# Performance work log

Hardware: AMD Instinct MI355X
Metric: run time of the kernel (lower is better)

## Reference

```python
import jax, jax.numpy as jnp
import numpy as np
from jax import lax

RATE = 2
KSIZE = 3
STRIDE = 1
FUSE_K = 3
SCALE = 10.0
DN = ('NCHW', 'OIHW', 'NCHW')


def extract_patches(x, k, s):
    # x: [B,C,H,W] -> [B,nH,nW,C,k,k]  (ZeroPad2d(1) when k != 1, as in torch code)
    B, C, H, W = x.shape
    p = 0 if k == 1 else 1
    xp = jnp.pad(x, ((0, 0), (0, 0), (p, p), (p, p)))
    nH = (H + 2 * p - k) // s + 1
    nW = (W + 2 * p - k) // s + 1
    cols = [xp[:, :, di:di + s * nH:s, dj:dj + s * nW:s]
            for di in range(k) for dj in range(k)]
    pat = jnp.stack(cols, 0).reshape(k, k, B, C, nH, nW)
    return pat.transpose(2, 4, 5, 3, 0, 1)


def _fuse(y):
    # conv of the [L,L] score image with eye(FUSE_K) kernel, same padding
    # == sum of diagonal shifts of the zero-padded image
    L = y.shape[0]
    p = (FUSE_K - 1) // 2
    A = jnp.pad(y, ((p, p), (p, p)))
    out = A[0:L, 0:L]
    for d in range(1, FUSE_K):
        out = out + A[d:d + L, d:d + L]
    return out


def _per_sample(xi, wi, raw_wi, mmi, h, w):
    # xi: [C,h,w]  wi: [L,C,3,3]  raw_wi: [L,C,4,4]  mmi: [L,1,1]
    L = h * w
    norm = jnp.sqrt(jnp.sum(wi * wi, axis=(1, 2, 3), keepdims=True))
    wi_n = wi / jnp.maximum(norm, 1e-4)
    # cosine-similarity conv: [L,h,w]
    yi = lax.conv_general_dilated(xi[None], wi_n, (1, 1), ((1, 1), (1, 1)),
                                  dimension_numbers=DN)[0]
    # fuse pass 1 on [L(patch), L(spatial)]
    y = _fuse(yi.reshape(L, L))
    # transpose (h_p,w_p,h',w') -> (w_p,h_p,w',h'), fuse pass 2, transpose back
    y = y.reshape(h, w, h, w).transpose(1, 0, 3, 2).reshape(L, L)
    y = _fuse(y)
    y = y.reshape(w, h, w, h).transpose(1, 0, 3, 2).reshape(L, h, w)
    y = y * mmi
    y = jax.nn.softmax(y * SCALE, axis=0)
    y = jnp.maximum(y * mmi, 1e-8)
    # conv_transpose2d(y, raw_wi, stride=2, padding=1) as lhs-dilated conv
    Wf = raw_wi[:, :, ::-1, ::-1].transpose(1, 0, 2, 3)  # [C,L,4,4]
    out = lax.conv_general_dilated(y[None], Wf, (1, 1), ((2, 2), (2, 2)),
                                   lhs_dilation=(2, 2),
                                   dimension_numbers=DN)[0]
    return out / 4.0


def reference(x1, x2, mask):
    B, C, H, W = x1.shape
    kernel = 2 * RATE
    raw_w = extract_patches(x1, kernel, RATE * STRIDE)
    x2s = x2[:, :, ::2, ::2]          # F.interpolate scale=0.5, nearest
    h, w = x2s.shape[2], x2s.shape[3]
    L = h * w
    raw_w = raw_w.reshape(B, L, C, kernel, kernel)
    wpat = extract_patches(x2s, KSIZE, STRIDE).reshape(B, L, C, KSIZE, KSIZE)
    # mask is already [B,1,h,w]: bilinear align_corners resize to (h,w) is identity
    m = extract_patches(mask, KSIZE, STRIDE).reshape(B, L, -1).mean(axis=2)
    mm = (m == 0.0).astype(x1.dtype)[:, :, None, None]  # [B,L,1,1]
    f = lambda xi, wi, rwi, mmi: _per_sample(xi, wi, rwi, mmi, h, w)
    return jax.vmap(f)(x2s, wpat, raw_w, mm)  # [B,C,H,W]


def setup_inputs() -> dict:
    key = jax.random.key(0)
    k1, k2 = jax.random.split(key)
    x1 = jax.random.normal(k1, (2, 128, 96, 96), dtype=jnp.float32)
    x2 = jax.random.normal(k2, (2, 128, 96, 96), dtype=jnp.float32)
    mask = jnp.zeros((2, 1, 48, 48), dtype=jnp.float32)
    return {"x1": x1, "x2": x2, "mask": mask}
```

## Files before the change

### kernel.cpp

```cpp
#include <hip/hip_runtime.h>
#include <hip/hip_bf16.h>

#define Cc   128
#define Hh   96
#define hs   48
#define Ls   2304
#define CK   2048
#define KG   384

typedef __attribute__((ext_vector_type(8))) short short8;
typedef __attribute__((ext_vector_type(4))) float f32x4;

__device__ __forceinline__ unsigned short f2bf(float x) {
    unsigned int u = __float_as_uint(x);
    unsigned int r = (u + 0x7fff + ((u >> 16) & 1)) >> 16;
    return (unsigned short)r;
}

__device__ __forceinline__ f32x4 ld4u(const float* p) {
    f32x4 v; __builtin_memcpy(&v, p, 16); return v;
}

#define GLOAD_LDS16(g, l) \
    __builtin_amdgcn_global_load_lds((__attribute__((address_space(1))) const void*)(g), \
                                     (__attribute__((address_space(3))) void*)(l), 16, 0, 0)


__global__ __launch_bounds__(256) void transposePQ_k(const float* __restrict__ x2,
                                                     unsigned short* __restrict__ P,
                                                     unsigned short* __restrict__ Q,
                                                     long long sPQ, int z0) {
    const int z = z0 + blockIdx.z;
    const float* x2b = x2 + (size_t)z * Cc * Hh * Hh;
    unsigned short* Pb = P + (size_t)blockIdx.z * sPQ;
    unsigned short* Qb = Q + (size_t)blockIdx.z * sPQ;
    __shared__ float tile[64][65];
    const int c0 = blockIdx.x * 64;
    const int l0 = blockIdx.y * 64;
    const int t = threadIdx.x;
    const int lt = t & 63, cg = t >> 6;
    const int l = l0 + lt;
    const int iy = l / hs, jx = l % hs;
    const int srcoff = iy * (2 * Hh) + 2 * jx;
#pragma unroll
    for (int cc = 0; cc < 16; ++cc) {
        int c = cg * 16 + cc;
        tile[lt][c] = x2b[(size_t)(c0 + c) * (Hh * Hh) + srcoff];
    }
    __syncthreads();
    const int lr = t >> 2, seg = t & 3;
    const int lw = l0 + lr;
    short8 hv0, hv1, lv0, lv1;
#pragma unroll
    for (int k = 0; k < 8; ++k) {
        float x = tile[lr][seg * 16 + k];
        unsigned short h = f2bf(x);
        float hf = __uint_as_float((unsigned)h << 16);
        unsigned short lo = f2bf(x - hf);
        hv0[k] = (short)h; lv0[k] = (short)lo;
    }
#pragma unroll
    for (int k = 0; k < 8; ++k) {
        float x = tile[lr][seg * 16 + 8 + k];
        unsigned short h = f2bf(x);
        float hf = __uint_as_float((unsigned)h << 16);
        unsigned short lo = f2bf(x - hf);
        hv1[k] = (short)h; lv1[k] = (short)lo;
    }
    size_t rowp = (size_t)lw * KG;
    int coff = c0 + seg * 16;
    *(short8*)&Pb[rowp + coff] = hv0;        *(short8*)&Pb[rowp + coff + 8] = hv1;
    *(short8*)&Pb[rowp + 128 + coff] = lv0;  *(short8*)&Pb[rowp + 128 + coff + 8] = lv1;
    *(short8*)&Pb[rowp + 256 + coff] = hv0;  *(short8*)&Pb[rowp + 256 + coff + 8] = hv1;
    *(short8*)&Qb[rowp + coff] = hv0;        *(short8*)&Qb[rowp + coff + 8] = hv1;
    *(short8*)&Qb[rowp + 128 + coff] = hv0;  *(short8*)&Qb[rowp + 128 + coff + 8] = hv1;
    *(short8*)&Qb[rowp + 256 + coff] = lv0;  *(short8*)&Qb[rowp + 256 + coff + 8] = lv1;
}

__global__ __launch_bounds__(256) void mm_k(const float* __restrict__ mask, float* __restrict__ MM) {
    int z = blockIdx.y;
    const float* mb = mask + (size_t)z * hs * hs;
    float* MMb = MM + (size_t)z * Ls;
    int l = blockIdx.x * 256 + threadIdx.x;
    if (l >= Ls) return;
    int ly = l / hs, lx = l % hs;
    float s = 0.f;
    for (int dy = -1; dy <= 1; ++dy)
        for (int dx = -1; dx <= 1; ++dx) {
            int yy = ly + dy, xx = lx + dx;
            if ((unsigned)yy < (unsigned)hs && (unsigned)xx < (unsigned)hs) s += mb[yy * hs + xx];
        }
    float m = s * (1.0f / 9.0f);
    MMb[l] = (m == 0.0f) ? 1.0f : 0.0f;
}

__global__ __launch_bounds__(256) void taps9rn_k(const float* __restrict__ G, float* __restrict__ S,
                                                 float* __restrict__ RN, long long zsG, long long zsS, int z0) {
    const float* Gb = G + (size_t)blockIdx.z * zsG;
    float* Sb = S + (size_t)blockIdx.z * zsS;
    float* RNb = RN + (size_t)(z0 + blockIdx.z) * Ls;
    int g = blockIdx.x * 256 + threadIdx.x;
    int i = g / 576;
    int jb = (g - i * 576) * 4;
    int iy = i / hs, ix = i % hs;
    int jy = jb / hs, jx0 = jb % hs;
    f32x4 acc = {};
#pragma unroll
    for (int dy = -1; dy <= 1; ++dy) {
        int vy = ((unsigned)(iy + dy) < (unsigned)hs) && ((unsigned)(jy + dy) < (unsigned)hs);
#pragma unroll
        for (int dx = -1; dx <= 1; ++dx) {
            int vi = vy && ((unsigned)(ix + dx) < (unsigned)hs);
            int o = hs * dy + dx;
            int row = vi ? (i + o) : i;
            f32x4 v = ld4u(&Gb[(size_t)row * Ls + jb + o]);
            f32x4 m;
#pragma unroll
            for (int ln = 0; ln < 4; ++ln)
                m[ln] = (vi && ((unsigned)(jx0 + ln + dx) < (unsigned)hs)) ? 1.f : 0.f;
            acc += v * m;
        }
    }
    __builtin_memcpy(&Sb[(size_t)i * Ls + jb], &acc, 16);
    int dd = i - jb;
    if ((unsigned)dd < 4u) RNb[i] = 1.0f / fmaxf(sqrtf(acc[dd]), 1e-4f);
}

__global__ __launch_bounds__(256) void fuse12T_k(const float* __restrict__ S, const float* __restrict__ RN,
                                                 float* __restrict__ ZT, long long zsS, long long zsZT, int z0) {
    const float* Sb = S + (size_t)blockIdx.z * zsS;
    float* ZTb = ZT + (size_t)blockIdx.z * zsZT;
    const float* RNb = RN + (size_t)(z0 + blockIdx.z) * Ls;
    __shared__ float tile[64][65];
    const int i0 = blockIdx.y * 64, j0 = blockIdx.x * 64;
    const int t = threadIdx.x;
    const int jg = t & 15, tit = t >> 4;
    const int jb = j0 + jg * 4;
    const int jy0 = jb / hs, jx0 = jb % hs;

    int ccb[9]; f32x4 m4[9];
#pragma unroll
    for (int d2 = -1; d2 <= 1; ++d2) {
        int cl[4], vb[4];
#pragma unroll
        for (int ln = 0; ln < 4; ++ln) {
            int j2 = (jx0 + ln) * hs + jy0 + d2;
            int vv = ((unsigned)j2 < (unsigned)Ls) ? 1 : 0;
            int c = vv ? ((j2 % hs) * hs + j2 / hs) : 0;
            cl[ln] = c; vb[ln] = vv;
        }
        int base = 0;
#pragma unroll
        for (int ln = 0; ln < 4; ++ln) if (vb[ln]) base = cl[ln] - ln;
#pragma unroll
        for (int d1 = -1; d1 <= 1; ++d1) {
            int idx = (d2 + 1) * 3 + (d1 + 1);
            ccb[idx] = base + d1;
            f32x4 mm;
#pragma unroll
            for (int ln = 0; ln < 4; ++ln) {
                int cc = cl[ln] + d1;
                mm[ln] = (vb[ln] && ((unsigned)cc < (unsigned)Ls)) ? 1.f : 0.f;
            }
            m4[idx] = mm;
        }
    }

    f32x4 acc[4] = {};
#pragma unroll
    for (int kk = 0; kk < 4; ++kk) {
        const int i = i0 + tit * 4 + kk;
        const int iy = i / hs, ix = i % hs;
        const int tif = ix * hs + iy;
#pragma unroll
        for (int d2 = -1; d2 <= 1; ++d2) {
            int i2 = tif + d2;
            int vi = ((unsigned)i2 < (unsigned)Ls) ? 1 : 0;
            int r = vi ? ((i2 % hs) * hs + i2 / hs) : 1;
#pragma unroll
            for (int d1 = -1; d1 <= 1; ++d1) {
                int rr = r + d1;
                int vr = vi && ((unsigned)rr < (unsigned)Ls);
                int rrc = vr ? rr : 0;
                float w = RNb[rrc];
                w = vr ? w : 0.f;
                int idx = (d2 + 1) * 3 + (d1 + 1);
                f32x4 v = ld4u(&Sb[(size_t)rrc * Ls + ccb[idx]]);
                acc[kk] += v * m4[idx] * w;
            }
        }
    }
#pragma unroll
    for (int kk = 0; kk < 4; ++kk) {
        int ti = tit * 4 + kk;
        tile[ti][jg * 4 + 0] = acc[kk][0];
        tile[ti][jg * 4 + 1] = acc[kk][1];
        tile[ti][jg * 4 + 2] = acc[kk][2];
        tile[ti][jg * 4 + 3] = acc[kk][3];
    }
    __syncthreads();
    const int r2 = t >> 2, cs = (t & 3) * 16;
    float vbuf[16];
#pragma unroll
    for (int k = 0; k < 16; ++k) vbuf[k] = tile[cs + k][r2];
    float* dst = &ZTb[(size_t)(j0 + r2) * Ls + i0 + cs];
#pragma unroll
    for (int k = 0; k < 4; ++k)
        *(float4*)&dst[k * 4] = *(float4*)&vbuf[k * 4];
}

__global__ __launch_bounds__(256) void softmax_row_k(const float* __restrict__ ZT, const float* __restrict__ MM,
                                                     unsigned short* __restrict__ AT, long long zsZT, int z0) {
    const int z = z0 + blockIdx.z;
    const float* ZTb = ZT + (size_t)blockIdx.z * zsZT;
    const float* MMb = MM + (size_t)z * Ls;
    unsigned short* ATb = AT + (size_t)z * Ls * Ls;
    const int w = threadIdx.x >> 6, lane = threadIdx.x & 63;
    const int p = blockIdx.x * 4 + w;
    const float* row = ZTb + (size_t)p * Ls;
    float v[36];
    float mx = -3.4e38f;
#pragma unroll
    for (int k = 0; k < 9; ++k) {
        const float4 zv = *(const float4*)&row[k * 256 + lane * 4];
        const float4 m = *(const float4*)&MMb[k * 256 + lane * 4];
        v[4 * k + 0] = zv.x * m.x * 10.f;
        v[4 * k + 1] = zv.y * m.y * 10.f;
        v[4 * k + 2] = zv.z * m.z * 10.f;
        v[4 * k + 3] = zv.w * m.w * 10.f;
        mx = fmaxf(mx, fmaxf(fmaxf(v[4 * k], v[4 * k + 1]), fmaxf(v[4 * k + 2], v[4 * k + 3])));
    }
#pragma unroll
    for (int off = 32; off; off >>= 1) mx = fmaxf(mx, __shfl_xor(mx, off));
    float sum = 0.f;
#pragma unroll
    for (int kk = 0; kk < 36; ++kk) { v[kk] = expf(v[kk] - mx); sum += v[kk]; }
#pragma unroll
    for (int off = 32; off; off >>= 1) sum += __shfl_xor(sum, off);
    const float rs = 1.0f / sum;
#pragma unroll
    for (int k = 0; k < 9; ++k) {
        const float4 m = *(const float4*)&MMb[k * 256 + lane * 4];
        ushort4 o;
        o.x = f2bf(fmaxf(v[4 * k + 0] * rs * m.x, 1e-8f));
        o.y = f2bf(fmaxf(v[4 * k + 1] * rs * m.y, 1e-8f));
        o.z = f2bf(fmaxf(v[4 * k + 2] * rs * m.z, 1e-8f));
        o.w = f2bf(fmaxf(v[4 * k + 3] * rs * m.w, 1e-8f));
        *(ushort4*)&ATb[(size_t)p * Ls + k * 256 + lane * 4] = o;
    }
}

__global__ __launch_bounds__(256) void gather_rwT_k(const float* __restrict__ x1, unsigned short* __restrict__ RWT) {
    const int z = blockIdx.z;
    const float* x1b = x1 + (size_t)z * Cc * Hh * Hh;
    unsigned short* R = RWT + (size_t)z * CK * Ls;
    int l = blockIdx.x * 256 + threadIdx.x;
    int ck = blockIdx.y;
    int c = ck >> 4, a = (ck >> 2) & 3, b2 = ck & 3;
    int ly = l / hs, lx = l % hs;
    int u = 2 * ly + a - 1, vv = 2 * lx + b2 - 1;
    float val = ((unsigned)u < (unsigned)Hh && (unsigned)vv < (unsigned)Hh) ? x1b[c * (Hh * Hh) + u * Hh + vv] : 0.0f;
    R[(size_t)ck * Ls + l] = f2bf(val);
}

__global__ __launch_bounds__(256) void scatter2_k(const float* __restrict__ T, float* __restrict__ out) {
    const int z = blockIdx.z;
    const int c = blockIdx.x;
    const float* Tb = T + (size_t)z * Ls * CK;
    float* outb = out + (size_t)z * Cc * Hh * Hh + (size_t)c * Hh * Hh;
    __shared__ float o[Hh * Hh];
    const int t = threadIdx.x;
    for (int i = t; i < Hh * Hh; i += 256) o[i] = 0.f;
    __syncthreads();
#pragma unroll
    for (int rep = 0; rep < 9; ++rep) {
        int p = rep * 256 + t;
        int i = p / hs, jj = p % hs;
        const float4* tp = (const float4*)&Tb[(size_t)p * CK + c * 16];
        float4 va = tp[0], vb = tp[1], vc = tp[2], vd = tp[3];
        float vals[16] = {va.x, va.y, va.z, va.w, vb.x, vb.y, vb.z, vb.w,
                          vc.x, vc.y, vc.z, vc.w, vd.x, vd.y, vd.z, vd.w};
#pragma unroll
        for (int a = 0; a < 4; ++a) {
            int Y = 2 * i + a - 1;
            if ((unsigned)Y >= (unsigned)Hh) continue;
#pragma unroll
            for (int b2 = 0; b2 < 4; ++b2) {
                int X = 2 * jj + b2 - 1;
                if ((unsigned)X >= (unsigned)Hh) continue;
                atomicAdd(&o[Y * Hh + X], vals[a * 4 + b2]);
            }
        }
    }
    __syncthreads();
    for (int i = t; i < Hh * Hh; i += 256) outb[i] = 0.25f * o[i];
}

__global__ __launch_bounds__(256) void mfma_gemm_k(const unsigned short* __restrict__ A,
                                                   const unsigned short* __restrict__ Bt,
                                                   float* __restrict__ C, int M, int N, int K,
                                                   long long sA, long long sB, long long sC,
                                                   int supertile) {
    A  += (size_t)blockIdx.z * sA;
    Bt += (size_t)blockIdx.z * sB;
    C  += (size_t)blockIdx.z * sC;

    const int nb = gridDim.x * gridDim.y;
    const int flat = blockIdx.y * gridDim.x + blockIdx.x;
    const int q = nb >> 3, r = nb & 7;
    const int xcd = flat & 7, sidx = flat >> 3;
    const int wg = (xcd < r ? xcd * (q + 1) : r * (q + 1) + (xcd - r) * q) + sidx;
    int bm, bn;
    if (supertile) {
        int st = wg / 12, tt = wg % 12;
        int stn = st & 3, stm = st >> 2;
        int tn = tt & 3, tm = tt >> 2;
        bn = (stn * 4 + tn) * 128;
        bm = (stm * 3 + tm) * 128;
    } else {
        bm = (wg / gridDim.x) * 128;
        bn = (wg % gridDim.x) * 128;
    }

    __shared__ __align__(16) unsigned short Asm[128 * 32];
    __shared__ __align__(16) unsigned short Bsm[128 * 32];
    const int t = threadIdx.x;
    const int lane = t & 63, w = t >> 6;
    const int wr = w >> 1, wc = w & 1;

    const int rA = 32 * w + (lane >> 2);
    const int kA = (lane & 3) * 8;
    const unsigned short* gA0 = A + (size_t)(bm + rA) * K + kA;
    const unsigned short* gA1 = gA0 + (size_t)16 * K;
    const unsigned short* gB0 = Bt + (size_t)(bn + rA) * K + kA;
    const unsigned short* gB1 = gB0 + (size_t)16 * K;
    unsigned short* lA0 = &Asm[(2 * w) * 512];
    unsigned short* lA1 = &Asm[(2 * w + 1) * 512];
    unsigned short* lB0 = &Bsm[(2 * w) * 512];
    unsigned short* lB1 = &Bsm[(2 * w + 1) * 512];

    const int fr = lane & 15, fq = lane >> 4;
    f32x4 acc[4][4] = {};

    for (int k0 = 0; k0 < K; k0 += 32) {
        GLOAD_LDS16(gA0 + k0, lA0);
        GLOAD_LDS16(gA1 + k0, lA1);
        GLOAD_LDS16(gB0 + k0, lB0);
        GLOAD_LDS16(gB1 + k0, lB1);
        __syncthreads();
        short8 av[4], bv[4];
#pragma unroll
        for (int m = 0; m < 4; ++m)
            av[m] = *(const short8*)&Asm[(wr * 64 + m * 16 + fr) * 32 + fq * 8];
#pragma unroll
        for (int n = 0; n < 4; ++n)
            bv[n] = *(const short8*)&Bsm[(wc * 64 + n * 16 + fr) * 32 + fq * 8];
#pragma unroll
        for (int m = 0; m < 4; ++m)
#pragma unroll
            for (int n = 0; n < 4; ++n)
                acc[m][n] = __builtin_amdgcn_mfma_f32_16x16x32_bf16(av[m], bv[n], acc[m][n], 0, 0, 0);
        __syncthreads();
    }
#pragma unroll
    for (int m = 0; m < 4; ++m) {
        int row0 = bm + wr * 64 + m * 16 + fq * 4;
#pragma unroll
        for (int n = 0; n < 4; ++n) {
            int col = bn + wc * 64 + n * 16 + fr;
#pragma unroll
            for (int rr = 0; rr < 4; ++rr)
                C[(size_t)(row0 + rr) * N + col] = acc[m][n][rr];
        }
    }
}


extern "C" void kernel_launch(void* const* d_in, const int* in_sizes, int n_in,
                              void* d_out, int out_size, void* d_ws, size_t ws_size,
                              hipStream_t stream) {
    const float* x1 = (const float*)d_in[0];
    const float* x2 = (const float*)d_in[1];
    const float* mask = (const float*)d_in[2];
    float* out = (float*)d_out;

    char* base = (char*)d_ws;
    const size_t LsLs = (size_t)Ls * Ls;
    const size_t LsCK = (size_t)Ls * CK;
    const long long sPQ = (long long)Ls * KG;

    const bool batched = ws_size >= 132175872ull;

    float* MM2 = (float*)(base);
    float* RN2 = (float*)(base + 20480);
    unsigned short *P, *Q, *ATb2, *RWT2;
    float *G, *S, *T2;
    if (batched) {
        P    = (unsigned short*)(base + 40960);
        Q    = (unsigned short*)(base + 3584000);
        G    = (float*)(base + 7127040);
        S    = (float*)(base + 49598464);
        ATb2 = (unsigned short*)(base + 92067840);
        RWT2 = (unsigned short*)(base + 113301504);
        T2   = (float*)base;
    } else {
        P    = (unsigned short*)(base + 40960);
        Q    = (unsigned short*)(base + 1812480);
        G    = (float*)(base + 3586048);
        S    = (float*)(base + 24823808);
        ATb2 = (unsigned short*)(base + 46059520);
        RWT2 = (unsigned short*)(base + 67293184);
        T2   = (float*)base;
    }

    mm_k<<<dim3(Ls / 256, 2), 256, 0, stream>>>(mask, MM2);
    gather_rwT_k<<<dim3(Ls / 256, CK, 2), 256, 0, stream>>>(x1, RWT2);

    const int tapsGrid = (Ls * 576) / 256;

    if (batched) {
        transposePQ_k<<<dim3(2, Ls / 64, 2), 256, 0, stream>>>(x2, P, Q, sPQ, 0);
        mfma_gemm_k<<<dim3(Ls / 128, Ls / 128, 2), 256, 0, stream>>>(
            P, Q, G, Ls, Ls, KG, sPQ, sPQ, (long long)LsLs, 0);
        taps9rn_k<<<dim3(tapsGrid, 1, 2), 256, 0, stream>>>(G, S, RN2, (long long)LsLs, (long long)LsLs, 0);
        fuse12T_k<<<dim3(Ls / 64, Ls / 64, 2), 256, 0, stream>>>(S, RN2, G, (long long)LsLs, (long long)LsLs, 0);
        softmax_row_k<<<dim3(Ls / 4, 1, 2), 256, 0, stream>>>(G, MM2, ATb2, (long long)LsLs, 0);
    } else {
        for (int z0 = 0; z0 < 2; ++z0) {
            transposePQ_k<<<dim3(2, Ls / 64, 1), 256, 0, stream>>>(x2, P, Q, 0, z0);
            mfma_gemm_k<<<dim3(Ls / 128, Ls / 128, 1), 256, 0, stream>>>(
                P, Q, G, Ls, Ls, KG, 0, 0, 0, 0);
            taps9rn_k<<<dim3(tapsGrid, 1, 1), 256, 0, stream>>>(G, S, RN2, 0, 0, z0);
            fuse12T_k<<<dim3(Ls / 64, Ls / 64, 1), 256, 0, stream>>>(S, RN2, G, 0, 0, z0);
            softmax_row_k<<<dim3(Ls / 4, 1, 1), 256, 0, stream>>>(G, MM2, ATb2, 0, z0);
        }
    }

    mfma_gemm_k<<<dim3(CK / 128, Ls / 128, 2), 256, 0, stream>>>(
        ATb2, RWT2, T2, Ls, CK, Ls,
        (long long)LsLs, (long long)LsCK, (long long)LsCK, 1);

    scatter2_k<<<dim3(Cc, 1, 2), 256, 0, stream>>>(T2, out);

    (void)in_sizes; (void)n_in; (void)out_size; (void)ws_size;
}
```

Measured before the change: 271.5 us.

## Double-buffer GEMM LDS tiles, store bf16 output, gather-based col2im scatter

The MFMA GEMM now uses two LDS buffers so the global-to-LDS load of the next K tile is issued while the current tile is being computed. It is templated so the second GEMM writes bf16 instead of fp32, which halves the size of the intermediate T buffer. The scatter kernel is rewritten as a gather: each block stages a bf16 slab of T in LDS and each output pixel sums its contributing taps directly, with no shared-memory atomics and with vector stores. Rounding T to bf16 adds precision loss, and the double buffer doubles the GEMM's LDS use.

```diff
diff --git a/kernel.cpp b/kernel.cpp
--- a/kernel.cpp
+++ b/kernel.cpp
@@ -15,6 +15,9 @@
     unsigned int u = __float_as_uint(x);
     unsigned int r = (u + 0x7fff + ((u >> 16) & 1)) >> 16;
     return (unsigned short)r;
+}
+__device__ __forceinline__ float bf2f(unsigned short h) {
+    return __uint_as_float((unsigned)h << 16);
 }
 
 __device__ __forceinline__ f32x4 ld4u(const float* p) {
@@ -263,47 +266,62 @@
     R[(size_t)ck * Ls + l] = f2bf(val);
 }
 
-__global__ __launch_bounds__(256) void scatter2_k(const float* __restrict__ T, float* __restrict__ out) {
+__global__ __launch_bounds__(256) void scatter3_k(const unsigned short* __restrict__ T, float* __restrict__ out) {
     const int z = blockIdx.z;
     const int c = blockIdx.x;
-    const float* Tb = T + (size_t)z * Ls * CK;
+    const int yh = blockIdx.y;
+    const unsigned short* Tb = T + (size_t)z * Ls * CK + (size_t)c * 16;
     float* outb = out + (size_t)z * Cc * Hh * Hh + (size_t)c * Hh * Hh;
-    __shared__ float o[Hh * Hh];
+    const int i0 = (yh == 0) ? 0 : 23;
+    __shared__ unsigned short Tl[1200 * 16];
     const int t = threadIdx.x;
-    for (int i = t; i < Hh * Hh; i += 256) o[i] = 0.f;
+#pragma unroll
+    for (int rep = 0; rep < 5; ++rep) {
+        int p = rep * 256 + t;
+        if (p < 1200)
+            __builtin_memcpy(&Tl[p * 16], &Tb[(size_t)(i0 * hs + p) * CK], 32);
+    }
     __syncthreads();
 #pragma unroll
-    for (int rep = 0; rep < 9; ++rep) {
-        int p = rep * 256 + t;
-        int i = p / hs, jj = p % hs;
-        const float4* tp = (const float4*)&Tb[(size_t)p * CK + c * 16];
-        float4 va = tp[0], vb = tp[1], vc = tp[2], vd = tp[3];
-        float vals[16] = {va.x, va.y, va.z, va.w, vb.x, vb.y, vb.z, vb.w,
-                          vc.x, vc.y, vc.z, vc.w, vd.x, vd.y, vd.z, vd.w};
-#pragma unroll
-        for (int a = 0; a < 4; ++a) {
-            int Y = 2 * i + a - 1;
-            if ((unsigned)Y >= (unsigned)Hh) continue;
-#pragma unroll
-            for (int b2 = 0; b2 < 4; ++b2) {
-                int X = 2 * jj + b2 - 1;
-                if ((unsigned)X >= (unsigned)Hh) continue;
-                atomicAdd(&o[Y * Hh + X], vals[a * 4 + b2]);
+    for (int rep = 0; rep < 5; ++rep) {
+        int idx4 = rep * 256 + t;
+        if (idx4 >= 1152) break;
+        int Y = yh * 48 + idx4 / 24;
+        int X0 = (idx4 % 24) * 4;
+        float o4[4];
+#pragma unroll
+        for (int xi = 0; xi < 4; ++xi) {
+            int X = X0 + xi;
+            int a0 = (Y + 1) & 1, b0 = (X + 1) & 1;
+            float s = 0.f;
+#pragma unroll
+            for (int ai = 0; ai < 2; ++ai) {
+                int a = a0 + 2 * ai;
+                int i = (Y + 1 - a) >> 1;
+                if ((unsigned)i >= (unsigned)hs) continue;
+#pragma unroll
+                for (int bi = 0; bi < 2; ++bi) {
+                    int b2 = b0 + 2 * bi;
+                    int jj = (X + 1 - b2) >> 1;
+                    if ((unsigned)jj >= (unsigned)hs) continue;
+                    s += bf2f(Tl[((i - i0) * hs + jj) * 16 + a * 4 + b2]);
+                }
             }
-        }
-    }
-    __syncthreads();
-    for (int i = t; i < Hh * Hh; i += 256) outb[i] = 0.25f * o[i];
-}
-
+            o4[xi] = 0.25f * s;
+        }
+        *(float4*)&outb[Y * Hh + X0] = *(float4*)&o4[0];
+    }
+}
+
+template <int SUPER, int CBF16>
 __global__ __launch_bounds__(256) void mfma_gemm_k(const unsigned short* __restrict__ A,
                                                    const unsigned short* __restrict__ Bt,
-                                                   float* __restrict__ C, int M, int N, int K,
-                                                   long long sA, long long sB, long long sC,
-                                                   int supertile) {
+                                                   void* __restrict__ Cv, int M, int N, int K,
+                                                   long long sA, long long sB, long long sC) {
     A  += (size_t)blockIdx.z * sA;
     Bt += (size_t)blockIdx.z * sB;
-    C  += (size_t)blockIdx.z * sC;
+    float* Cf = (float*)Cv + (CBF16 ? 0 : (size_t)blockIdx.z * sC);
+    unsigned short* Ch = (unsigned short*)Cv + (CBF16 ? (size_t)blockIdx.z * sC : 0);
 
     const int nb = gridDim.x * gridDim.y;
     const int flat = blockIdx.y * gridDim.x + blockIdx.x;
@@ -311,7 +329,7 @@
     const int xcd = flat & 7, sidx = flat >> 3;
     const int wg = (xcd < r ? xcd * (q + 1) : r * (q + 1) + (xcd - r) * q) + sidx;
     int bm, bn;
-    if (supertile) {
+    if (SUPER) {
         int st = wg / 12, tt = wg % 12;
         int stn = st & 3, stm = st >> 2;
         int tn = tt & 3, tm = tt >> 2;
@@ -322,8 +340,8 @@
         bn = (wg % gridDim.x) * 128;
     }
 
-    __shared__ __align__(16) unsigned short Asm[128 * 32];
-    __shared__ __align__(16) unsigned short Bsm[128 * 32];
+    __shared__ __align__(16) unsigned short Asm[2][128 * 32];
+    __shared__ __align__(16) unsigned short Bsm[2][128 * 32];
     const int t = threadIdx.x;
     const int lane = t & 63, w = t >> 6;
     const int wr = w >> 1, wc = w & 1;
@@ -334,34 +352,40 @@
     const unsigned short* gA1 = gA0 + (size_t)16 * K;
     const unsigned short* gB0 = Bt + (size_t)(bn + rA) * K + kA;
     const unsigned short* gB1 = gB0 + (size_t)16 * K;
-    unsigned short* lA0 = &Asm[(2 * w) * 512];
-    unsigned short* lA1 = &Asm[(2 * w + 1) * 512];
-    unsigned short* lB0 = &Bsm[(2 * w) * 512];
-    unsigned short* lB1 = &Bsm[(2 * w + 1) * 512];
+
+#define STAGE4(b, koff) do { \
+        GLOAD_LDS16(gA0 + (koff), &Asm[b][(2 * w) * 512]); \
+        GLOAD_LDS16(gA1 + (koff), &Asm[b][(2 * w + 1) * 512]); \
+        GLOAD_LDS16(gB0 + (koff), &Bsm[b][(2 * w) * 512]); \
+        GLOAD_LDS16(gB1 + (koff), &Bsm[b][(2 * w + 1) * 512]); \
+    } while (0)
 
     const int fr = lane & 15, fq = lane >> 4;
     f32x4 acc[4][4] = {};
 
-    for (int k0 = 0; k0 < K; k0 += 32) {
-        GLOAD_LDS16(gA0 + k0, lA0);
-        GLOAD_LDS16(gA1 + k0, lA1);
-        GLOAD_LDS16(gB0 + k0, lB0);
-        GLOAD_LDS16(gB1 + k0, lB1);
-        __syncthreads();
+    const int nt = K >> 5;
+    STAGE4(0, 0);
+    __syncthreads();
+    int cur = 0;
+    for (int tt = 0; tt < nt; ++tt) {
+        if (tt + 1 < nt) STAGE4(cur ^ 1, (tt + 1) * 32);
         short8 av[4], bv[4];
 #pragma unroll
         for (int m = 0; m < 4; ++m)
-            av[m] = *(const short8*)&Asm[(wr * 64 + m * 16 + fr) * 32 + fq * 8];
+            av[m] = *(const short8*)&Asm[cur][(wr * 64 + m * 16 + fr) * 32 + fq * 8];
 #pragma unroll
         for (int n = 0; n < 4; ++n)
-            bv[n] = *(const short8*)&Bsm[(wc * 64 + n * 16 + fr) * 32 + fq * 8];
+            bv[n] = *(const short8*)&Bsm[cur][(wc * 64 + n * 16 + fr) * 32 + fq * 8];
 #pragma unroll
         for (int m = 0; m < 4; ++m)
 #pragma unroll
             for (int n = 0; n < 4; ++n)
                 acc[m][n] = __builtin_amdgcn_mfma_f32_16x16x32_bf16(av[m], bv[n], acc[m][n], 0, 0, 0);
         __syncthreads();
-    }
+        cur ^= 1;
+    }
+#undef STAGE4
+
 #pragma unroll
     for (int m = 0; m < 4; ++m) {
         int row0 = bm + wr * 64 + m * 16 + fq * 4;
@@ -369,8 +393,12 @@
         for (int n = 0; n < 4; ++n) {
             int col = bn + wc * 64 + n * 16 + fr;
 #pragma unroll
-            for (int rr = 0; rr < 4; ++rr)
-                C[(size_t)(row0 + rr) * N + col] = acc[m][n][rr];
+            for (int rr = 0; rr < 4; ++rr) {
+                if (CBF16)
+                    Ch[(size_t)(row0 + rr) * N + col] = f2bf(acc[m][n][rr]);
+                else
+                    Cf[(size_t)(row0 + rr) * N + col] = acc[m][n][rr];
+            }
         }
     }
 }
@@ -394,7 +422,8 @@
     float* MM2 = (float*)(base);
     float* RN2 = (float*)(base + 20480);
     unsigned short *P, *Q, *ATb2, *RWT2;
-    float *G, *S, *T2;
+    float *G, *S;
+    unsigned short* T2 = (unsigned short*)base;
     if (batched) {
         P    = (unsigned short*)(base + 40960);
         Q    = (unsigned short*)(base + 3584000);
@@ -402,7 +431,6 @@
         S    = (float*)(base + 49598464);
         ATb2 = (unsigned short*)(base + 92067840);
         RWT2 = (unsigned short*)(base + 113301504);
-        T2   = (float*)base;
     } else {
         P    = (unsigned short*)(base + 40960);
         Q    = (unsigned short*)(base + 1812480);
@@ -410,7 +438,6 @@
         S    = (float*)(base + 24823808);
         ATb2 = (unsigned short*)(base + 46059520);
         RWT2 = (unsigned short*)(base + 67293184);
-        T2   = (float*)base;
     }
 
     mm_k<<<dim3(Ls / 256, 2), 256, 0, stream>>>(mask, MM2);
@@ -420,27 +447,27 @@
 
     if (batched) {
         transposePQ_k<<<dim3(2, Ls / 64, 2), 256, 0, stream>>>(x2, P, Q, sPQ, 0);
-        mfma_gemm_k<<<dim3(Ls / 128, Ls / 128, 2), 256, 0, stream>>>(
-            P, Q, G, Ls, Ls, KG, sPQ, sPQ, (long long)LsLs, 0);
+        mfma_gemm_k<0, 0><<<dim3(Ls / 128, Ls / 128, 2), 256, 0, stream>>>(
+            P, Q, G, Ls, Ls, KG, sPQ, sPQ, (long long)LsLs);
         taps9rn_k<<<dim3(tapsGrid, 1, 2), 256, 0, stream>>>(G, S, RN2, (long long)LsLs, (long long)LsLs, 0);
         fuse12T_k<<<dim3(Ls / 64, Ls / 64, 2), 256, 0, stream>>>(S, RN2, G, (long long)LsLs, (long long)LsLs, 0);
         softmax_row_k<<<dim3(Ls / 4, 1, 2), 256, 0, stream>>>(G, MM2, ATb2, (long long)LsLs, 0);
     } else {
         for (int z0 = 0; z0 < 2; ++z0) {
             transposePQ_k<<<dim3(2, Ls / 64, 1), 256, 0, stream>>>(x2, P, Q, 0, z0);
-            mfma_gemm_k<<<dim3(Ls / 128, Ls / 128, 1), 256, 0, stream>>>(
-                P, Q, G, Ls, Ls, KG, 0, 0, 0, 0);
+            mfma_gemm_k<0, 0><<<dim3(Ls / 128, Ls / 128, 1), 256, 0, stream>>>(
+                P, Q, G, Ls, Ls, KG, 0, 0, 0);
             taps9rn_k<<<dim3(tapsGrid, 1, 1), 256, 0, stream>>>(G, S, RN2, 0, 0, z0);
             fuse12T_k<<<dim3(Ls / 64, Ls / 64, 1), 256, 0, stream>>>(S, RN2, G, 0, 0, z0);
             softmax_row_k<<<dim3(Ls / 4, 1, 1), 256, 0, stream>>>(G, MM2, ATb2, 0, z0);
         }
     }
 
-    mfma_gemm_k<<<dim3(CK / 128, Ls / 128, 2), 256, 0, stream>>>(
+    mfma_gemm_k<1, 1><<<dim3(CK / 128, Ls / 128, 2), 256, 0, stream>>>(
         ATb2, RWT2, T2, Ls, CK, Ls,
-        (long long)LsLs, (long long)LsCK, (long long)LsCK, 1);
-
-    scatter2_k<<<dim3(Cc, 1, 2), 256, 0, stream>>>(T2, out);
+        (long long)LsLs, (long long)LsCK, (long long)LsCK);
+
+    scatter3_k<<<dim3(Cc, 2, 2), 256, 0, stream>>>(T2, out);
 
     (void)in_sizes; (void)n_in; (void)out_size; (void)ws_size;
 }
```

After: 223.8 us. 1.21x faster.
